# Performance work log

Measured on AMD Instinct MI355X. Metric: run time of the kernel, lower is better.

The kernel has to match this reference:

```python
import jax, jax.numpy as jnp
import numpy as np

TEMPERATURE = 8.0  # sqrt(d_k) with d_k=64

def setup_inputs() -> dict:
    key = jax.random.key(0)
    k1, k2, k3, k4 = jax.random.split(key, 4)
    B, L, D = 64, 1024, 64  # B = batch*n_heads
    q = jax.random.normal(k1, (B, L, D), dtype=jnp.float32)
    k = jax.random.normal(k2, (B, L, D), dtype=jnp.float32)
    v = jax.random.normal(k3, (B, L, D), dtype=jnp.float32)
    mask = jax.random.randint(k4, (B, L, L), 0, 2).astype(jnp.bool_)
    return {"q": q, "k": k, "v": v, "mask": mask}

def reference(q, k, v, mask):
    # scores: [B, Lq, Lk]
    attn = jnp.einsum('bqd,bkd->bqk', q, k) / TEMPERATURE
    attn = jnp.where(mask, -jnp.inf, attn)
    attn = jax.nn.softmax(attn, axis=2)
    output = jnp.einsum('bqk,bkd->bqd', attn, v)
    return (output, attn)
```

## Files before the change

kernel.cpp:

```cpp
#include <hip/hip_runtime.h>

#define B_ 64
#define L_ 1024
#define D_ 64
#define QT 16

typedef _Float16 f16;
typedef __attribute__((ext_vector_type(8))) _Float16 f16x8;
typedef __attribute__((ext_vector_type(4))) float f32x4;

#define WS_KH 0u
#define WS_KL 8388608u
#define WS_VT 16777216u
#define WS_NEED 25165824u

__device__ __forceinline__ int sidx(int row, int col) {
    return row * 1024 + ((((col >> 3) ^ (row & 7)) << 3) | (col & 7));
}


__global__ __launch_bounds__(256)
void prep_k(const float* __restrict__ kk, f16* __restrict__ kh, f16* __restrict__ kl) {
    const int i = (blockIdx.x * 256 + threadIdx.x) * 8;
    float4 f0 = *(const float4*)(kk + i);
    float4 f1 = *(const float4*)(kk + i + 4);
    float fv[8] = {f0.x, f0.y, f0.z, f0.w, f1.x, f1.y, f1.z, f1.w};
    f16x8 h, lo;
    #pragma unroll
    for (int j = 0; j < 8; ++j) {
        float x = fv[j] * 0.125f;
        f16 hh = (f16)x;
        h[j] = hh;
        lo[j] = (f16)(x - (float)hh);
    }
    *(f16x8*)(kh + i) = h;
    *(f16x8*)(kl + i) = lo;
}

__global__ __launch_bounds__(256)
void prep_v(const float* __restrict__ v, f16* __restrict__ vt) {
    __shared__ f16 tile[64][72];
    const int b = blockIdx.x >> 4, kt = blockIdx.x & 15;
    const int r = threadIdx.x >> 2, c0 = (threadIdx.x & 3) * 16;
    const float* vp = v + (size_t)(b * L_ + kt * 64 + r) * D_ + c0;
    float4 g0 = *(const float4*)vp;
    float4 g1 = *(const float4*)(vp + 4);
    float4 g2 = *(const float4*)(vp + 8);
    float4 g3 = *(const float4*)(vp + 12);
    float fv[16] = {g0.x, g0.y, g0.z, g0.w, g1.x, g1.y, g1.z, g1.w,
                    g2.x, g2.y, g2.z, g2.w, g3.x, g3.y, g3.z, g3.w};
    #pragma unroll
    for (int j = 0; j < 16; ++j) tile[r][c0 + j] = (f16)fv[j];
    __syncthreads();
    f16x8 o0, o1;
    #pragma unroll
    for (int j = 0; j < 8; ++j) { o0[j] = tile[c0 + j][r]; o1[j] = tile[c0 + 8 + j][r]; }
    f16* op = vt + (size_t)(b * 64 + r) * 1024 + kt * 64 + c0;
    *(f16x8*)op = o0;
    *(f16x8*)(op + 8) = o1;
}


__global__ __launch_bounds__(256, 4)
void sdpa_main(const float* __restrict__ q, const f16* __restrict__ kh,
               const f16* __restrict__ kl, const f16* __restrict__ vt,
               const unsigned char* __restrict__ mask,
               float* __restrict__ out, float* __restrict__ attn)
{
    __shared__ __align__(16) char smem[QT * 1024 * 2];
    __shared__ float wsumP[4][QT];
    f16* S = (f16*)smem;
    float* OL = (float*)smem;

    const int tid = threadIdx.x;
    const int l = tid & 63, w = tid >> 6;
    const int lr = l & 15, lg = l >> 4;
    const int bid = blockIdx.x;
    const int b = bid >> 6, qt = bid & 63;
    const int qbase = b * L_ + qt * QT;

    unsigned det = 0;
    {
        const unsigned* mw = (const unsigned*)mask;
        #pragma unroll
        for (int i = 0; i < 32; ++i) det |= mw[i];
    }
    const bool elem4 = (det <= 1u) || (det == 0x3F800000u);

    f16x8 aqh[2], aql[2];
    {
        const float* qp = q + (size_t)(qbase + lr) * D_;
        #pragma unroll
        for (int s = 0; s < 2; ++s) {
            float4 f0 = *(const float4*)(qp + s * 32 + lg * 8);
            float4 f1 = *(const float4*)(qp + s * 32 + lg * 8 + 4);
            float fv[8] = {f0.x, f0.y, f0.z, f0.w, f1.x, f1.y, f1.z, f1.w};
            #pragma unroll
            for (int j = 0; j < 8; ++j) {
                f16 h = (f16)fv[j];
                aqh[s][j] = h;
                aql[s][j] = (f16)(fv[j] - (float)h);
            }
        }
    }

    const f16* khp = kh + (size_t)(b * L_ + w * 16 + lr) * D_ + lg * 8;
    const f16* klp = kl + (size_t)(b * L_ + w * 16 + lr) * D_ + lg * 8;
    const size_t mrowbase = (size_t)(qbase + lg * 4) * L_ + w * 16 + lr;

    f16x8 bhc[2], blc[2];
    bhc[0] = *(const f16x8*)khp;  bhc[1] = *(const f16x8*)(khp + 32);
    blc[0] = *(const f16x8*)klp;  blc[1] = *(const f16x8*)(klp + 32);
    int mcur[4], mnxt[4];
    #pragma unroll
    for (int r2 = 0; r2 < 4; ++r2) {
        if (elem4) {
            mcur[r2] = ((const int*)mask)[mrowbase + (size_t)r2 * L_];
            mnxt[r2] = ((const int*)mask)[mrowbase + (size_t)r2 * L_ + 64];
        } else {
            mcur[r2] = mask[mrowbase + (size_t)r2 * L_];
            mnxt[r2] = mask[mrowbase + (size_t)r2 * L_ + 64];
        }
    }

    float vsum[4] = {0.f, 0.f, 0.f, 0.f};
    for (int ck = 0; ck < 16; ++ck) {
        f16x8 bhn[2], bln[2];
        if (ck < 15) {
            const f16* p1 = khp + (size_t)(ck + 1) * 64 * D_;
            const f16* p2 = klp + (size_t)(ck + 1) * 64 * D_;
            bhn[0] = *(const f16x8*)p1; bhn[1] = *(const f16x8*)(p1 + 32);
            bln[0] = *(const f16x8*)p2; bln[1] = *(const f16x8*)(p2 + 32);
        }
        int mfut[4];
        if (ck < 14) {
            const size_t mo = mrowbase + (size_t)(ck + 2) * 64;
            if (elem4) {
                #pragma unroll
                for (int r2 = 0; r2 < 4; ++r2) mfut[r2] = ((const int*)mask)[mo + (size_t)r2 * L_];
            } else {
                #pragma unroll
                for (int r2 = 0; r2 < 4; ++r2) mfut[r2] = mask[mo + (size_t)r2 * L_];
            }
        }
        f32x4 acc = {0.f, 0.f, 0.f, 0.f};
        #pragma unroll
        for (int s = 0; s < 2; ++s) {
            acc = __builtin_amdgcn_mfma_f32_16x16x32_f16(aqh[s], bhc[s], acc, 0, 0, 0);
            acc = __builtin_amdgcn_mfma_f32_16x16x32_f16(aql[s], bhc[s], acc, 0, 0, 0);
            acc = __builtin_amdgcn_mfma_f32_16x16x32_f16(aqh[s], blc[s], acc, 0, 0, 0);
        }
        const int scol = ck * 64 + w * 16 + lr;
        #pragma unroll
        for (int r2 = 0; r2 < 4; ++r2) {
            float e = mcur[r2] ? 0.f : __expf(acc[r2]);
            S[sidx(lg * 4 + r2, scol)] = (f16)e;
            vsum[r2] += e;
        }
        #pragma unroll
        for (int r2 = 0; r2 < 4; ++r2) mcur[r2] = mnxt[r2];
        if (ck < 14) {
            #pragma unroll
            for (int r2 = 0; r2 < 4; ++r2) mnxt[r2] = mfut[r2];
        }
        if (ck < 15) {
            #pragma unroll
            for (int s = 0; s < 2; ++s) { bhc[s] = bhn[s]; blc[s] = bln[s]; }
        }
    }
    #pragma unroll
    for (int r2 = 0; r2 < 4; ++r2) {
        #pragma unroll
        for (int off = 1; off < 16; off <<= 1)
            vsum[r2] += __shfl_xor(vsum[r2], off);
    }
    if (lr == 0) {
        #pragma unroll
        for (int r2 = 0; r2 < 4; ++r2) wsumP[w][lg * 4 + r2] = vsum[r2];
    }
    __syncthreads();

    const float inv = 1.0f / (wsumP[0][lr] + wsumP[1][lr] + wsumP[2][lr] + wsumP[3][lr]);
    const int kq = w * 256;
    const f16* vtb = vt + (size_t)b * 64 * 1024 + kq + lg * 8;
    float* ap = attn + (size_t)(qbase + lr) * L_ + kq + lg * 8;

    f32x4 acc4[4] = {{0,0,0,0},{0,0,0,0},{0,0,0,0},{0,0,0,0}};
    f16x8 bv[4], bvn[4];
    #pragma unroll
    for (int nt = 0; nt < 4; ++nt)
        bv[nt] = *(const f16x8*)(vtb + (size_t)(nt * 16 + lr) * 1024);

    for (int t = 0; t < 8; ++t) {
        if (t < 7) {
            #pragma unroll
            for (int nt = 0; nt < 4; ++nt)
                bvn[nt] = *(const f16x8*)(vtb + (size_t)(nt * 16 + lr) * 1024 + (t + 1) * 32);
        }
        f16x8 e8 = *(const f16x8*)&S[sidx(lr, kq + t * 32 + lg * 8)];
        f32x4 p0, p1;
        p0[0] = (float)e8[0] * inv; p0[1] = (float)e8[1] * inv;
        p0[2] = (float)e8[2] * inv; p0[3] = (float)e8[3] * inv;
        p1[0] = (float)e8[4] * inv; p1[1] = (float)e8[5] * inv;
        p1[2] = (float)e8[6] * inv; p1[3] = (float)e8[7] * inv;
        *(f32x4*)(ap + t * 32)     = p0;
        *(f32x4*)(ap + t * 32 + 4) = p1;
        #pragma unroll
        for (int nt = 0; nt < 4; ++nt)
            acc4[nt] = __builtin_amdgcn_mfma_f32_16x16x32_f16(e8, bv[nt], acc4[nt], 0, 0, 0);
        if (t < 7) {
            #pragma unroll
            for (int nt = 0; nt < 4; ++nt) bv[nt] = bvn[nt];
        }
    }
    __syncthreads();

    #pragma unroll
    for (int nt = 0; nt < 4; ++nt) {
        #pragma unroll
        for (int r2 = 0; r2 < 4; ++r2)
            OL[w * (16 * 68) + (lg * 4 + r2) * 68 + nt * 16 + lr] = acc4[nt][r2];
    }
    __syncthreads();
    {
        const int row = tid >> 4, c4 = (tid & 15) * 4;
        f32x4 o = {0.f, 0.f, 0.f, 0.f};
        #pragma unroll
        for (int ww = 0; ww < 4; ++ww) {
            const float* p = &OL[ww * (16 * 68) + row * 68 + c4];
            o[0] += p[0]; o[1] += p[1]; o[2] += p[2]; o[3] += p[3];
        }
        const float invr = 1.0f / (wsumP[0][row] + wsumP[1][row] + wsumP[2][row] + wsumP[3][row]);
        f32x4 r = {o[0] * invr, o[1] * invr, o[2] * invr, o[3] * invr};
        *(f32x4*)(out + (size_t)(qbase + row) * D_ + c4) = r;
    }
}


__global__ __launch_bounds__(256, 4)
void sdpa_fallback(const float* __restrict__ q, const float* __restrict__ kk,
                   const float* __restrict__ v, const unsigned char* __restrict__ mask,
                   float* __restrict__ out, float* __restrict__ attn)
{
    __shared__ f16 S[QT * 1024];
    __shared__ float wmax[4][QT];
    __shared__ float wsum[QT];

    const int tid = threadIdx.x;
    const int l = tid & 63, w = tid >> 6;
    const int lr = l & 15, lg = l >> 4;
    const int bid = blockIdx.x;
    const int b = bid >> 6, qt = bid & 63;
    const int qbase = b * L_ + qt * QT;

    unsigned det = 0;
    {
        const unsigned* mw = (const unsigned*)mask;
        #pragma unroll
        for (int i = 0; i < 32; ++i) det |= mw[i];
    }
    const bool elem4 = (det <= 1u) || (det == 0x3F800000u);

    f16x8 aqh[2], aql[2];
    {
        const float* qp = q + (size_t)(qbase + lr) * D_;
        #pragma unroll
        for (int s = 0; s < 2; ++s) {
            float4 f0 = *(const float4*)(qp + s * 32 + lg * 8);
            float4 f1 = *(const float4*)(qp + s * 32 + lg * 8 + 4);
            float fv[8] = {f0.x, f0.y, f0.z, f0.w, f1.x, f1.y, f1.z, f1.w};
            #pragma unroll
            for (int j = 0; j < 8; ++j) {
                f16 h = (f16)fv[j];
                aqh[s][j] = h;
                aql[s][j] = (f16)(fv[j] - (float)h);
            }
        }
    }

    float vmax[4] = {-INFINITY, -INFINITY, -INFINITY, -INFINITY};
    const float* kb = kk + (size_t)(b * L_ + w * 16 + lr) * D_ + lg * 8;
    const size_t mrowbase = (size_t)(qbase + lg * 4) * L_ + w * 16 + lr;

    float4 kc[4];
    kc[0] = *(const float4*)kb;
    kc[1] = *(const float4*)(kb + 4);
    kc[2] = *(const float4*)(kb + 32);
    kc[3] = *(const float4*)(kb + 36);
    int mcur[4], mnxt[4];
    #pragma unroll
    for (int r2 = 0; r2 < 4; ++r2) {
        if (elem4) {
            mcur[r2] = ((const int*)mask)[mrowbase + (size_t)r2 * L_];
            mnxt[r2] = ((const int*)mask)[mrowbase + (size_t)r2 * L_ + 64];
        } else {
            mcur[r2] = mask[mrowbase + (size_t)r2 * L_];
            mnxt[r2] = mask[mrowbase + (size_t)r2 * L_ + 64];
        }
    }

    for (int ck = 0; ck < 16; ++ck) {
        float4 kn[4];
        if (ck < 15) {
            const float* kp = kb + (size_t)(ck + 1) * 64 * D_;
            kn[0] = *(const float4*)kp;
            kn[1] = *(const float4*)(kp + 4);
            kn[2] = *(const float4*)(kp + 32);
            kn[3] = *(const float4*)(kp + 36);
        }
        int mfut[4];
        if (ck < 14) {
            const size_t mo = mrowbase + (size_t)(ck + 2) * 64;
            if (elem4) {
                #pragma unroll
                for (int r2 = 0; r2 < 4; ++r2) mfut[r2] = ((const int*)mask)[mo + (size_t)r2 * L_];
            } else {
                #pragma unroll
                for (int r2 = 0; r2 < 4; ++r2) mfut[r2] = mask[mo + (size_t)r2 * L_];
            }
        }
        f16x8 bh[2], bl[2];
        #pragma unroll
        for (int s = 0; s < 2; ++s) {
            float fv[8] = {kc[2*s].x, kc[2*s].y, kc[2*s].z, kc[2*s].w,
                           kc[2*s+1].x, kc[2*s+1].y, kc[2*s+1].z, kc[2*s+1].w};
            #pragma unroll
            for (int j = 0; j < 8; ++j) {
                f16 h = (f16)fv[j];
                bh[s][j] = h;
                bl[s][j] = (f16)(fv[j] - (float)h);
            }
        }
        f32x4 acc = {0.f, 0.f, 0.f, 0.f};
        #pragma unroll
        for (int s = 0; s < 2; ++s) {
            acc = __builtin_amdgcn_mfma_f32_16x16x32_f16(aqh[s], bh[s], acc, 0, 0, 0);
            acc = __builtin_amdgcn_mfma_f32_16x16x32_f16(aql[s], bh[s], acc, 0, 0, 0);
            acc = __builtin_amdgcn_mfma_f32_16x16x32_f16(aqh[s], bl[s], acc, 0, 0, 0);
        }
        const int scol = ck * 64 + w * 16 + lr;
        #pragma unroll
        for (int r2 = 0; r2 < 4; ++r2) {
            float sv = mcur[r2] ? -INFINITY : acc[r2] * 0.125f;
            S[sidx(lg * 4 + r2, scol)] = (f16)sv;
            vmax[r2] = fmaxf(vmax[r2], sv);
        }
        #pragma unroll
        for (int r2 = 0; r2 < 4; ++r2) mcur[r2] = mnxt[r2];
        if (ck < 14) {
            #pragma unroll
            for (int r2 = 0; r2 < 4; ++r2) mnxt[r2] = mfut[r2];
        }
        if (ck < 15) {
            #pragma unroll
            for (int j = 0; j < 4; ++j) kc[j] = kn[j];
        }
    }
    #pragma unroll
    for (int r2 = 0; r2 < 4; ++r2) {
        #pragma unroll
        for (int off = 1; off < 16; off <<= 1)
            vmax[r2] = fmaxf(vmax[r2], __shfl_xor(vmax[r2], off));
    }
    if (lr == 0) {
        #pragma unroll
        for (int r2 = 0; r2 < 4; ++r2) wmax[w][lg * 4 + r2] = vmax[r2];
    }
    __syncthreads();

    {
        const int row = tid >> 4, cg = tid & 15;
        const float m = fmaxf(fmaxf(wmax[0][row], wmax[1][row]),
                              fmaxf(wmax[2][row], wmax[3][row]));
        float sum = 0.f;
        #pragma unroll
        for (int c = 0; c < 8; ++c) {
            f16* sp = &S[row * 1024 + (((cg + 16 * c) ^ (row & 7)) << 3)];
            f16x8 sv = *(const f16x8*)sp;
            f16x8 ev;
            #pragma unroll
            for (int j = 0; j < 8; ++j) {
                float e = __expf((float)sv[j] - m);
                ev[j] = (f16)e;
                sum += e;
            }
            *(f16x8*)sp = ev;
        }
        #pragma unroll
        for (int off = 1; off < 16; off <<= 1) sum += __shfl_xor(sum, off);
        if (cg == 0) wsum[row] = sum;
        __syncthreads();

        const float inv = 1.0f / wsum[row];
        float* ap = attn + (size_t)(qbase + row) * L_;
        #pragma unroll
        for (int c = 0; c < 8; ++c) {
            f16x8 ev = *(const f16x8*)&S[row * 1024 + (((cg + 16 * c) ^ (row & 7)) << 3)];
            float4 p0, p1;
            p0.x = (float)ev[0] * inv; p0.y = (float)ev[1] * inv;
            p0.z = (float)ev[2] * inv; p0.w = (float)ev[3] * inv;
            p1.x = (float)ev[4] * inv; p1.y = (float)ev[5] * inv;
            p1.z = (float)ev[6] * inv; p1.w = (float)ev[7] * inv;
            *(float4*)(ap + (cg + 16 * c) * 8)     = p0;
            *(float4*)(ap + (cg + 16 * c) * 8 + 4) = p1;
        }
    }

    f32x4 acc2 = {0.f, 0.f, 0.f, 0.f};
    const float* vb = v + (size_t)(b * L_) * D_ + w * 16 + lr;
    float vcA[8], vcB[8];
    #pragma unroll
    for (int j = 0; j < 8; ++j) {
        vcA[j] = vb[(size_t)(lg * 8 + j) * D_];
        vcB[j] = vb[(size_t)(32 + lg * 8 + j) * D_];
    }
    for (int tt = 0; tt < 16; ++tt) {
        {
            f16x8 pa = *(const f16x8*)&S[lr * 1024 + ((((2 * tt) * 4 + lg) ^ (lr & 7)) << 3)];
            f16x8 bv;
            #pragma unroll
            for (int j = 0; j < 8; ++j) bv[j] = (f16)vcA[j];
            if (tt < 15) {
                const float* vp = vb + (size_t)((2 * tt + 2) * 32 + lg * 8) * D_;
                #pragma unroll
                for (int j = 0; j < 8; ++j) vcA[j] = vp[(size_t)j * D_];
            }
            acc2 = __builtin_amdgcn_mfma_f32_16x16x32_f16(pa, bv, acc2, 0, 0, 0);
        }
        {
            f16x8 pa = *(const f16x8*)&S[lr * 1024 + ((((2 * tt + 1) * 4 + lg) ^ (lr & 7)) << 3)];
            f16x8 bv;
            #pragma unroll
            for (int j = 0; j < 8; ++j) bv[j] = (f16)vcB[j];
            if (tt < 15) {
                const float* vp = vb + (size_t)((2 * tt + 3) * 32 + lg * 8) * D_;
                #pragma unroll
                for (int j = 0; j < 8; ++j) vcB[j] = vp[(size_t)j * D_];
            }
            acc2 = __builtin_amdgcn_mfma_f32_16x16x32_f16(pa, bv, acc2, 0, 0, 0);
        }
    }

    #pragma unroll
    for (int r2 = 0; r2 < 4; ++r2) {
        const float invr = 1.0f / wsum[lg * 4 + r2];
        out[(size_t)(qbase + lg * 4 + r2) * D_ + w * 16 + lr] = acc2[r2] * invr;
    }
}

extern "C" void kernel_launch(void* const* d_in, const int* in_sizes, int n_in,
                              void* d_out, int out_size, void* d_ws, size_t ws_size,
                              hipStream_t stream) {
    const float* q = (const float*)d_in[0];
    const float* k = (const float*)d_in[1];
    const float* v = (const float*)d_in[2];
    const unsigned char* mask = (const unsigned char*)d_in[3];
    float* out = (float*)d_out;
    float* attn = out + (size_t)B_ * L_ * D_;

    if (ws_size >= (size_t)WS_NEED) {
        f16* kh = (f16*)((char*)d_ws + WS_KH);
        f16* kl = (f16*)((char*)d_ws + WS_KL);
        f16* vt = (f16*)((char*)d_ws + WS_VT);
        prep_k<<<dim3(2048), 256, 0, stream>>>(k, kh, kl);
        prep_v<<<dim3(1024), 256, 0, stream>>>(v, vt);
        sdpa_main<<<dim3(B_ * (L_ / QT)), 256, 0, stream>>>(q, kh, kl, vt, mask, out, attn);
    } else {
        sdpa_fallback<<<dim3(B_ * (L_ / QT)), 256, 0, stream>>>(q, k, v, mask, out, attn);
    }
}
```

Before: 278.2 us.

## Load mask coalesced in softmax phase, fuse K/V prep kernels, unroll PV loop

```diff
diff --git a/kernel.cpp b/kernel.cpp
--- a/kernel.cpp
+++ b/kernel.cpp
@@ -18,46 +18,46 @@
     return row * 1024 + ((((col >> 3) ^ (row & 7)) << 3) | (col & 7));
 }
 
-
 __global__ __launch_bounds__(256)
-void prep_k(const float* __restrict__ kk, f16* __restrict__ kh, f16* __restrict__ kl) {
-    const int i = (blockIdx.x * 256 + threadIdx.x) * 8;
-    float4 f0 = *(const float4*)(kk + i);
-    float4 f1 = *(const float4*)(kk + i + 4);
-    float fv[8] = {f0.x, f0.y, f0.z, f0.w, f1.x, f1.y, f1.z, f1.w};
-    f16x8 h, lo;
-    #pragma unroll
-    for (int j = 0; j < 8; ++j) {
-        float x = fv[j] * 0.125f;
-        f16 hh = (f16)x;
-        h[j] = hh;
-        lo[j] = (f16)(x - (float)hh);
-    }
-    *(f16x8*)(kh + i) = h;
-    *(f16x8*)(kl + i) = lo;
-}
-
-__global__ __launch_bounds__(256)
-void prep_v(const float* __restrict__ v, f16* __restrict__ vt) {
+void prep_kv(const float* __restrict__ kk, const float* __restrict__ v,
+             f16* __restrict__ kh, f16* __restrict__ kl, f16* __restrict__ vt) {
     __shared__ f16 tile[64][72];
-    const int b = blockIdx.x >> 4, kt = blockIdx.x & 15;
-    const int r = threadIdx.x >> 2, c0 = (threadIdx.x & 3) * 16;
-    const float* vp = v + (size_t)(b * L_ + kt * 64 + r) * D_ + c0;
-    float4 g0 = *(const float4*)vp;
-    float4 g1 = *(const float4*)(vp + 4);
-    float4 g2 = *(const float4*)(vp + 8);
-    float4 g3 = *(const float4*)(vp + 12);
-    float fv[16] = {g0.x, g0.y, g0.z, g0.w, g1.x, g1.y, g1.z, g1.w,
-                    g2.x, g2.y, g2.z, g2.w, g3.x, g3.y, g3.z, g3.w};
-    #pragma unroll
-    for (int j = 0; j < 16; ++j) tile[r][c0 + j] = (f16)fv[j];
-    __syncthreads();
-    f16x8 o0, o1;
-    #pragma unroll
-    for (int j = 0; j < 8; ++j) { o0[j] = tile[c0 + j][r]; o1[j] = tile[c0 + 8 + j][r]; }
-    f16* op = vt + (size_t)(b * 64 + r) * 1024 + kt * 64 + c0;
-    *(f16x8*)op = o0;
-    *(f16x8*)(op + 8) = o1;
+    if (blockIdx.x < 2048) {
+        const int i = (blockIdx.x * 256 + threadIdx.x) * 8;
+        float4 f0 = *(const float4*)(kk + i);
+        float4 f1 = *(const float4*)(kk + i + 4);
+        float fv[8] = {f0.x, f0.y, f0.z, f0.w, f1.x, f1.y, f1.z, f1.w};
+        f16x8 h, lo;
+        #pragma unroll
+        for (int j = 0; j < 8; ++j) {
+            float x = fv[j] * 0.125f;
+            f16 hh = (f16)x;
+            h[j] = hh;
+            lo[j] = (f16)(x - (float)hh);
+        }
+        *(f16x8*)(kh + i) = h;
+        *(f16x8*)(kl + i) = lo;
+    } else {
+        const int bb = blockIdx.x - 2048;
+        const int b = bb >> 4, kt = bb & 15;
+        const int r = threadIdx.x >> 2, c0 = (threadIdx.x & 3) * 16;
+        const float* vp = v + (size_t)(b * L_ + kt * 64 + r) * D_ + c0;
+        float4 g0 = *(const float4*)vp;
+        float4 g1 = *(const float4*)(vp + 4);
+        float4 g2 = *(const float4*)(vp + 8);
+        float4 g3 = *(const float4*)(vp + 12);
+        float fv[16] = {g0.x, g0.y, g0.z, g0.w, g1.x, g1.y, g1.z, g1.w,
+                        g2.x, g2.y, g2.z, g2.w, g3.x, g3.y, g3.z, g3.w};
+        #pragma unroll
+        for (int j = 0; j < 16; ++j) tile[r][c0 + j] = (f16)fv[j];
+        __syncthreads();
+        f16x8 o0, o1;
+        #pragma unroll
+        for (int j = 0; j < 8; ++j) { o0[j] = tile[c0 + j][r]; o1[j] = tile[c0 + 8 + j][r]; }
+        f16* op = vt + (size_t)(b * 64 + r) * 1024 + kt * 64 + c0;
+        *(f16x8*)op = o0;
+        *(f16x8*)(op + 8) = o1;
+    }
 }
 
 
@@ -106,24 +106,11 @@
 
     const f16* khp = kh + (size_t)(b * L_ + w * 16 + lr) * D_ + lg * 8;
     const f16* klp = kl + (size_t)(b * L_ + w * 16 + lr) * D_ + lg * 8;
-    const size_t mrowbase = (size_t)(qbase + lg * 4) * L_ + w * 16 + lr;
 
     f16x8 bhc[2], blc[2];
     bhc[0] = *(const f16x8*)khp;  bhc[1] = *(const f16x8*)(khp + 32);
     blc[0] = *(const f16x8*)klp;  blc[1] = *(const f16x8*)(klp + 32);
-    int mcur[4], mnxt[4];
-    #pragma unroll
-    for (int r2 = 0; r2 < 4; ++r2) {
-        if (elem4) {
-            mcur[r2] = ((const int*)mask)[mrowbase + (size_t)r2 * L_];
-            mnxt[r2] = ((const int*)mask)[mrowbase + (size_t)r2 * L_ + 64];
-        } else {
-            mcur[r2] = mask[mrowbase + (size_t)r2 * L_];
-            mnxt[r2] = mask[mrowbase + (size_t)r2 * L_ + 64];
-        }
-    }
-
-    float vsum[4] = {0.f, 0.f, 0.f, 0.f};
+
     for (int ck = 0; ck < 16; ++ck) {
         f16x8 bhn[2], bln[2];
         if (ck < 15) {
@@ -132,17 +119,6 @@
             bhn[0] = *(const f16x8*)p1; bhn[1] = *(const f16x8*)(p1 + 32);
             bln[0] = *(const f16x8*)p2; bln[1] = *(const f16x8*)(p2 + 32);
         }
-        int mfut[4];
-        if (ck < 14) {
-            const size_t mo = mrowbase + (size_t)(ck + 2) * 64;
-            if (elem4) {
-                #pragma unroll
-                for (int r2 = 0; r2 < 4; ++r2) mfut[r2] = ((const int*)mask)[mo + (size_t)r2 * L_];
-            } else {
-                #pragma unroll
-                for (int r2 = 0; r2 < 4; ++r2) mfut[r2] = mask[mo + (size_t)r2 * L_];
-            }
-        }
         f32x4 acc = {0.f, 0.f, 0.f, 0.f};
         #pragma unroll
         for (int s = 0; s < 2; ++s) {
@@ -153,67 +129,81 @@
         const int scol = ck * 64 + w * 16 + lr;
         #pragma unroll
         for (int r2 = 0; r2 < 4; ++r2) {
-            float e = mcur[r2] ? 0.f : __expf(acc[r2]);
-            S[sidx(lg * 4 + r2, scol)] = (f16)e;
-            vsum[r2] += e;
-        }
-        #pragma unroll
-        for (int r2 = 0; r2 < 4; ++r2) mcur[r2] = mnxt[r2];
-        if (ck < 14) {
-            #pragma unroll
-            for (int r2 = 0; r2 < 4; ++r2) mnxt[r2] = mfut[r2];
+            S[sidx(lg * 4 + r2, scol)] = (f16)__expf(acc[r2]);
         }
         if (ck < 15) {
             #pragma unroll
             for (int s = 0; s < 2; ++s) { bhc[s] = bhn[s]; blc[s] = bln[s]; }
         }
     }
-    #pragma unroll
-    for (int r2 = 0; r2 < 4; ++r2) {
-        #pragma unroll
-        for (int off = 1; off < 16; off <<= 1)
-            vsum[r2] += __shfl_xor(vsum[r2], off);
-    }
-    if (lr == 0) {
-        #pragma unroll
-        for (int r2 = 0; r2 < 4; ++r2) wsumP[w][lg * 4 + r2] = vsum[r2];
-    }
     __syncthreads();
 
+    const int kq = w * 256;
+
+    f16x8 e0 = *(const f16x8*)&S[sidx(lr, kq + 0 * 32 + lg * 8)];
+    f16x8 e1 = *(const f16x8*)&S[sidx(lr, kq + 1 * 32 + lg * 8)];
+    f16x8 e2 = *(const f16x8*)&S[sidx(lr, kq + 2 * 32 + lg * 8)];
+    f16x8 e3 = *(const f16x8*)&S[sidx(lr, kq + 3 * 32 + lg * 8)];
+    f16x8 e4 = *(const f16x8*)&S[sidx(lr, kq + 4 * 32 + lg * 8)];
+    f16x8 e5 = *(const f16x8*)&S[sidx(lr, kq + 5 * 32 + lg * 8)];
+    f16x8 e6 = *(const f16x8*)&S[sidx(lr, kq + 6 * 32 + lg * 8)];
+    f16x8 e7 = *(const f16x8*)&S[sidx(lr, kq + 7 * 32 + lg * 8)];
+
+    const size_t moff = (size_t)(qbase + lr) * L_ + kq + lg * 8;
+    float rsum = 0.f;
+    #define APPLY_MASK(ET, T)                                                  \
+    {                                                                          \
+        int mm[8];                                                             \
+        if (elem4) {                                                           \
+            int4 a = *(const int4*)((const int*)mask + moff + (T) * 32);       \
+            int4 c = *(const int4*)((const int*)mask + moff + (T) * 32 + 4);   \
+            mm[0]=a.x; mm[1]=a.y; mm[2]=a.z; mm[3]=a.w;                        \
+            mm[4]=c.x; mm[5]=c.y; mm[6]=c.z; mm[7]=c.w;                        \
+        } else {                                                               \
+            uchar4 a = *(const uchar4*)(mask + moff + (T) * 32);               \
+            uchar4 c = *(const uchar4*)(mask + moff + (T) * 32 + 4);           \
+            mm[0]=a.x; mm[1]=a.y; mm[2]=a.z; mm[3]=a.w;                        \
+            mm[4]=c.x; mm[5]=c.y; mm[6]=c.z; mm[7]=c.w;                        \
+        }                                                                      \
+        _Pragma("unroll")                                                      \
+        for (int j = 0; j < 8; ++j) {                                          \
+            ET[j] = mm[j] ? (f16)0.f : ET[j];                                  \
+            rsum += (float)ET[j];                                              \
+        }                                                                      \
+    }
+    APPLY_MASK(e0, 0) APPLY_MASK(e1, 1) APPLY_MASK(e2, 2) APPLY_MASK(e3, 3)
+    APPLY_MASK(e4, 4) APPLY_MASK(e5, 5) APPLY_MASK(e6, 6) APPLY_MASK(e7, 7)
+    #undef APPLY_MASK
+
+    rsum += __shfl_xor(rsum, 16);
+    rsum += __shfl_xor(rsum, 32);
+    if (l < 16) wsumP[w][lr] = rsum;
+    __syncthreads();
+
     const float inv = 1.0f / (wsumP[0][lr] + wsumP[1][lr] + wsumP[2][lr] + wsumP[3][lr]);
-    const int kq = w * 256;
+
+    float* ap = attn + moff;
     const f16* vtb = vt + (size_t)b * 64 * 1024 + kq + lg * 8;
-    float* ap = attn + (size_t)(qbase + lr) * L_ + kq + lg * 8;
-
     f32x4 acc4[4] = {{0,0,0,0},{0,0,0,0},{0,0,0,0},{0,0,0,0}};
-    f16x8 bv[4], bvn[4];
-    #pragma unroll
-    for (int nt = 0; nt < 4; ++nt)
-        bv[nt] = *(const f16x8*)(vtb + (size_t)(nt * 16 + lr) * 1024);
-
-    for (int t = 0; t < 8; ++t) {
-        if (t < 7) {
-            #pragma unroll
-            for (int nt = 0; nt < 4; ++nt)
-                bvn[nt] = *(const f16x8*)(vtb + (size_t)(nt * 16 + lr) * 1024 + (t + 1) * 32);
-        }
-        f16x8 e8 = *(const f16x8*)&S[sidx(lr, kq + t * 32 + lg * 8)];
-        f32x4 p0, p1;
-        p0[0] = (float)e8[0] * inv; p0[1] = (float)e8[1] * inv;
-        p0[2] = (float)e8[2] * inv; p0[3] = (float)e8[3] * inv;
-        p1[0] = (float)e8[4] * inv; p1[1] = (float)e8[5] * inv;
-        p1[2] = (float)e8[6] * inv; p1[3] = (float)e8[7] * inv;
-        *(f32x4*)(ap + t * 32)     = p0;
-        *(f32x4*)(ap + t * 32 + 4) = p1;
-        #pragma unroll
-        for (int nt = 0; nt < 4; ++nt)
-            acc4[nt] = __builtin_amdgcn_mfma_f32_16x16x32_f16(e8, bv[nt], acc4[nt], 0, 0, 0);
-        if (t < 7) {
-            #pragma unroll
-            for (int nt = 0; nt < 4; ++nt) bv[nt] = bvn[nt];
-        }
-    }
-    __syncthreads();
+
+    #define STEP(ET, T)                                                        \
+    {                                                                          \
+        f32x4 p0, p1;                                                          \
+        p0[0] = (float)ET[0] * inv; p0[1] = (float)ET[1] * inv;                \
+        p0[2] = (float)ET[2] * inv; p0[3] = (float)ET[3] * inv;                \
+        p1[0] = (float)ET[4] * inv; p1[1] = (float)ET[5] * inv;                \
+        p1[2] = (float)ET[6] * inv; p1[3] = (float)ET[7] * inv;                \
+        *(f32x4*)(ap + (T) * 32)     = p0;                                     \
+        *(f32x4*)(ap + (T) * 32 + 4) = p1;                                     \
+        _Pragma("unroll")                                                      \
+        for (int nt = 0; nt < 4; ++nt) {                                       \
+            f16x8 bv = *(const f16x8*)(vtb + (size_t)(nt * 16 + lr) * 1024 + (T) * 32); \
+            acc4[nt] = __builtin_amdgcn_mfma_f32_16x16x32_f16(ET, bv, acc4[nt], 0, 0, 0); \
+        }                                                                      \
+    }
+    STEP(e0, 0) STEP(e1, 1) STEP(e2, 2) STEP(e3, 3)
+    STEP(e4, 4) STEP(e5, 5) STEP(e6, 6) STEP(e7, 7)
+    #undef STEP
 
     #pragma unroll
     for (int nt = 0; nt < 4; ++nt) {
@@ -462,8 +452,7 @@
         f16* kh = (f16*)((char*)d_ws + WS_KH);
         f16* kl = (f16*)((char*)d_ws + WS_KL);
         f16* vt = (f16*)((char*)d_ws + WS_VT);
-        prep_k<<<dim3(2048), 256, 0, stream>>>(k, kh, kl);
-        prep_v<<<dim3(1024), 256, 0, stream>>>(v, vt);
+        prep_kv<<<dim3(3072), 256, 0, stream>>>(k, v, kh, kl, vt);
         sdpa_main<<<dim3(B_ * (L_ / QT)), 256, 0, stream>>>(q, kh, kl, vt, mask, out, attn);
     } else {
         sdpa_fallback<<<dim3(B_ * (L_ / QT)), 256, 0, stream>>>(q, k, v, mask, out, attn);
```

After: 274.9 us. About the same (-1.2%).
